# Kernel tuning notes

Hardware: AMD Instinct MI355X
Metric: run time of the kernel (lower is better)

## Reference

```python
import jax, jax.numpy as jnp
import numpy as np

NUM_NODES, NUM_RELS = 100000, 32
VOCAB = NUM_NODES + NUM_RELS
EMB, HID, LAYERS, CW = 128, 768, 4, 3
NHEAD, HDIM = HID // 64, 64
B, S = 4, 1024
T = S - 4 * CW  # rows where the full banded submask fits
EPS = 1e-5


def setup_inputs() -> dict:
    key = jax.random.key(0)
    ks = jax.random.split(key, 24)
    f32 = jnp.float32
    d = {}
    d["seq"] = jax.random.randint(ks[0], (B, S), 0, VOCAB)
    d["neg_ids"] = jax.random.randint(ks[1], (T, B), 0, VOCAB)
    # embedding + LayerNorm
    d["emb_table"] = jax.random.normal(ks[2], (VOCAB, EMB), f32)
    d["emb_ln_g"] = jnp.ones((EMB,), f32)
    d["emb_ln_b"] = jnp.zeros((EMB,), f32)
    # proj: Linear(EMB->HID) + GELU
    d["proj_w"] = jax.random.normal(ks[3], (HID, EMB), f32) * 0.02
    d["proj_b"] = jnp.zeros((HID,), f32)
    # transformer encoder layers (torch post-norm layout)
    d["wqkv"] = jax.random.normal(ks[4], (LAYERS, 3 * HID, HID), f32) * 0.02
    d["bqkv"] = jnp.zeros((LAYERS, 3 * HID), f32)
    d["wo"] = jax.random.normal(ks[5], (LAYERS, HID, HID), f32) * 0.02
    d["bo"] = jnp.zeros((LAYERS, HID), f32)
    d["ln1_g"] = jnp.ones((LAYERS, HID), f32)
    d["ln1_b"] = jnp.zeros((LAYERS, HID), f32)
    d["w1"] = jax.random.normal(ks[6], (LAYERS, 4 * HID, HID), f32) * 0.02
    d["b1"] = jnp.zeros((LAYERS, 4 * HID), f32)
    d["w2"] = jax.random.normal(ks[7], (LAYERS, HID, 4 * HID), f32) * 0.02
    d["b2"] = jnp.zeros((LAYERS, HID), f32)
    d["ln2_g"] = jnp.ones((LAYERS, HID), f32)
    d["ln2_b"] = jnp.zeros((LAYERS, HID), f32)
    # out: Linear(HID->EMB) + LayerNorm
    d["out_w"] = jax.random.normal(ks[8], (EMB, HID), f32) * 0.02
    d["out_b"] = jnp.zeros((EMB,), f32)
    d["out_ln_g"] = jnp.ones((EMB,), f32)
    d["out_ln_b"] = jnp.zeros((EMB,), f32)
    return d


def _ln(x, g, b):
    m = x.mean(-1, keepdims=True)
    v = x.var(-1, keepdims=True)
    return (x - m) * jax.lax.rsqrt(v + EPS) * g + b


def _pos_encoding(s, h):
    pos = jnp.arange(s, dtype=jnp.float32)[:, None]
    div = jnp.exp(jnp.arange(0, h, 2, dtype=jnp.float32) * (-jnp.log(10000.0) / h))
    ang = pos * div  # (S, H/2)
    pe = jnp.zeros((s, h), jnp.float32)
    pe = pe.at[:, 0::2].set(jnp.sin(ang)).at[:, 1::2].set(jnp.cos(ang))
    return pe[:, None, :]  # (S,1,H)


def _band_mask(s):
    i = jnp.arange(s)[:, None]
    j = jnp.arange(s)[None, :]
    gap = j - i
    allowed = (gap >= 0) & (gap <= 4 * CW) & (gap != 2 * CW)
    return jnp.where(allowed, 0.0, -jnp.inf).astype(jnp.float32)


def reference(seq, neg_ids, emb_table, emb_ln_g, emb_ln_b, proj_w, proj_b,
              wqkv, bqkv, wo, bo, ln1_g, ln1_b, w1, b1, w2, b2, ln2_g, ln2_b,
              out_w, out_b, out_ln_g, out_ln_b):
    seq_t = seq.T  # (S,B)
    s, b = seq_t.shape
    z = _ln(emb_table[seq_t], emb_ln_g, emb_ln_b)                 # (S,B,EMB)
    tokens = jax.nn.gelu(jnp.einsum('sbe,he->sbh', z, proj_w) + proj_b,
                         approximate=False)                        # (S,B,HID)
    tokens = tokens + _pos_encoding(s, HID)
    mask = _band_mask(s)                                           # (S,S)
    scale = 1.0 / jnp.sqrt(jnp.float32(HDIM))
    x = tokens
    for l in range(LAYERS):
        qkv = jnp.einsum('sbh,gh->sbg', x, wqkv[l]) + bqkv[l]      # (S,B,3H)
        q, k, v = [t.reshape(s, b, NHEAD, HDIM)
                   for t in jnp.split(qkv, 3, axis=-1)]
        scores = jnp.einsum('sbhd,tbhd->bhst', q, k) * scale + mask
        a = jax.nn.softmax(scores, axis=-1)                        # (B,H,S,S)
        attn = jnp.einsum('bhst,tbhd->sbhd', a, v).reshape(s, b, HID)
        attn = jnp.einsum('sbh,gh->sbg', attn, wo[l]) + bo[l]
        x = _ln(x + attn, ln1_g[l], ln1_b[l])
        ff = jax.nn.gelu(jnp.einsum('sbh,fh->sbf', x, w1[l]) + b1[l],
                         approximate=False)
        ff = jnp.einsum('sbf,hf->sbh', ff, w2[l]) + b2[l]
        x = _ln(x + ff, ln2_g[l], ln2_b[l])
    z_out = _ln(jnp.einsum('sbh,eh->sbe', x, out_w) + out_b,
                out_ln_g, out_ln_b)                                # (S,B,EMB)
    targets = jnp.arange(T) + CW + 1                               # (T,)
    z_hat = z_out[targets]                                         # (T,B,EMB)
    z_pos = z[targets]
    pos = jnp.sum(z_pos * z_hat, axis=-1).reshape(-1)              # (T*B,)
    z_neg = _ln(emb_table[neg_ids], emb_ln_g, emb_ln_b)            # (T,B,EMB)
    neg = jnp.sum(z_neg * z_hat, axis=-1).reshape(-1)              # (T*B,)
    # BCEWithLogitsLoss: labels 1 for pos, 0 for neg
    loss = (jnp.sum(jax.nn.softplus(-pos)) + jnp.sum(jax.nn.softplus(neg))) \
           / (pos.size + neg.size)
    return loss
```

## Files before the change

kernel.cpp:

```cpp
#include <hip/hip_runtime.h>
#include <hip/hip_bf16.h>
#include <math.h>

#define S_LEN 1024
#define B_DIM 4
#define EMB 128
#define HID 768
#define LAYERS 4
#define CW 3
#define NHEAD 12
#define HDIM 64
#define T_LEN (S_LEN - 4*CW)
#define LN_EPS 1e-5f
#define MROWS (S_LEN*B_DIM)

typedef unsigned short u16;
typedef __attribute__((ext_vector_type(8))) __bf16 bf16x8;
typedef __attribute__((ext_vector_type(4))) float f32x4;

__device__ __forceinline__ u16 f2b(float f){
    unsigned u = __float_as_uint(f);
    u += 0x7fff + ((u >> 16) & 1);
    return (u16)(u >> 16);
}
__device__ __forceinline__ float b2f(u16 h){
    return __uint_as_float(((unsigned)h) << 16);
}
__device__ __forceinline__ float gelu_exact(float x){
    return 0.5f * x * (1.0f + erff(x * 0.70710678118654752f));
}
__device__ __forceinline__ float softplus_f(float x){
    return fmaxf(x, 0.0f) + log1pf(expf(-fabsf(x)));
}
template<int N> __device__ __forceinline__ void waitcnt_vm(){
    if constexpr(N==0) asm volatile("s_waitcnt vmcnt(0)" ::: "memory");
    else if constexpr(N==2) asm volatile("s_waitcnt vmcnt(2)" ::: "memory");
    else if constexpr(N==3) asm volatile("s_waitcnt vmcnt(3)" ::: "memory");
    else if constexpr(N==4) asm volatile("s_waitcnt vmcnt(4)" ::: "memory");
    else if constexpr(N==6) asm volatile("s_waitcnt vmcnt(6)" ::: "memory");
    else if constexpr(N==8) asm volatile("s_waitcnt vmcnt(8)" ::: "memory");
}

__global__ void k_cvt(const float* __restrict__ w, u16* __restrict__ o, int n4){
    int i = blockIdx.x*256 + threadIdx.x;
    if(i >= n4) return;
    float4 v = *(const float4*)(w + (size_t)i*4);
    ushort4 t; t.x=f2b(v.x); t.y=f2b(v.y); t.z=f2b(v.z); t.w=f2b(v.w);
    *(ushort4*)(o + (size_t)i*4) = t;
}

__global__ void k_pe(float* __restrict__ pe){
    int idx = blockIdx.x*256 + threadIdx.x;
    if(idx >= S_LEN*HID) return;
    int s = idx / HID, c = idx % HID;
    int i2 = (c >> 1) * 2;
    float freq = expf(-(float)i2 * (logf(10000.0f) / (float)HID));
    float ang = (float)s * freq;
    pe[idx] = (c & 1) ? cosf(ang) : sinf(ang);
}

__global__ void k_embed_ln(const int* __restrict__ seq,
                           const float* __restrict__ emb,
                           const float* __restrict__ g,
                           const float* __restrict__ bta,
                           float* __restrict__ z, u16* __restrict__ zb){
    int row = blockIdx.x;
    int s = row >> 2, b = row & 3;
    int tok = seq[b*S_LEN + s];
    const float* e = emb + (size_t)tok * EMB;
    int lane = threadIdx.x;
    float v0 = e[lane], v1 = e[lane+64];
    float sum = v0+v1, sq = v0*v0+v1*v1;
    #pragma unroll
    for(int off=32; off; off>>=1){ sum += __shfl_xor(sum,off); sq += __shfl_xor(sq,off); }
    float m = sum * (1.0f/128.0f);
    float var = sq*(1.0f/128.0f) - m*m;
    float r = rsqrtf(var + LN_EPS);
    size_t base = (size_t)row*EMB;
    float o0 = (v0-m)*r*g[lane]    + bta[lane];
    float o1 = (v1-m)*r*g[lane+64] + bta[lane+64];
    z[base+lane] = o0; z[base+lane+64] = o1;
    zb[base+lane] = f2b(o0); zb[base+lane+64] = f2b(o1);
}

template<int BM, int BN, int THR, int EPI, int WF, int WB>
__global__ __launch_bounds__(THR) void k_mm(
    const u16*  __restrict__ A,
    const u16*  __restrict__ Bw,
    const float* __restrict__ bias,
    float* __restrict__ Cf, u16* __restrict__ Cb,
    int M, int N, int K, const float* __restrict__ pe)
{
    constexpr int WCOL = (THR==512) ? 4 : 2;
    constexpr int WM = BM/2, WN = BN/WCOL, MR = WM/16, NR = WN/16;
    constexpr int RA = (BM*4)/THR;
    constexpr int RB = (BN*4)/THR;
    constexpr int IC = RA + RB;
    static_assert(RA >= 1 && RB >= 1, "tile too small for THR");
    __shared__ u16 Al[3][BM*32];
    __shared__ u16 Bl[3][BN*32];
    int tid = threadIdx.x;
    int wave = tid >> 6, lane = tid & 63;

    int nbx = N / BN, nby = M / BM, nwg = nbx * nby;
    int bid = blockIdx.x;
    int q = nwg >> 3, rm = nwg & 7, xcd = bid & 7, off = bid >> 3;
    int sbid = (xcd < rm ? xcd*(q+1) : rm*(q+1) + (xcd-rm)*q) + off;
    int row0 = (sbid / nbx) * BM, col0 = (sbid % nbx) * BN;

    int wr = wave / WCOL, wc = wave % WCOL;
    int lr = lane & 15, lk = lane >> 4;

    f32x4 acc[MR][NR];
    #pragma unroll
    for(int m=0;m<MR;m++)
        #pragma unroll
        for(int n=0;n<NR;n++) acc[m][n] = (f32x4){0.f,0.f,0.f,0.f};

    const char* Abase = (const char*)A;
    const char* Bbase = (const char*)Bw;

    auto stage = [&](int buf, int k0){
        #pragma unroll
        for(int i=0;i<RA;i++){
            int p = i*(THR*16) + tid*16;
            int rr = p >> 6, u = (p >> 4) & 3;
            int us = u ^ ((rr >> 1) & 3);
            const char* g = Abase + ((size_t)(row0+rr)*K + k0)*2 + us*16;
            void* l = (char*)&Al[buf][0] + i*(THR*16) + wave*1024;
            __builtin_amdgcn_global_load_lds(
                (const __attribute__((address_space(1))) void*)g,
                (__attribute__((address_space(3))) void*)l, 16, 0, 0);
        }
        #pragma unroll
        for(int i=0;i<RB;i++){
            int p = i*(THR*16) + tid*16;
            int rr = p >> 6, u = (p >> 4) & 3;
            int us = u ^ ((rr >> 1) & 3);
            const char* g = Bbase + ((size_t)(col0+rr)*K + k0)*2 + us*16;
            void* l = (char*)&Bl[buf][0] + i*(THR*16) + wave*1024;
            __builtin_amdgcn_global_load_lds(
                (const __attribute__((address_space(1))) void*)g,
                (__attribute__((address_space(3))) void*)l, 16, 0, 0);
        }
    };

    int nt = K >> 5;
    stage(0, 0);
    if(nt > 1) stage(1, 32);
    int cur = 0;
    for(int t=0; t<nt; ++t){
        int pre = (cur==0) ? 2 : cur-1;
        if(t+2 < nt) stage(pre, (t+2) << 5);
        if(t+2 < nt)      waitcnt_vm<2*IC>();
        else if(t+1 < nt) waitcnt_vm<IC>();
        else              waitcnt_vm<0>();
        __builtin_amdgcn_s_barrier();
        __builtin_amdgcn_sched_barrier(0);
        bf16x8 af[MR], bfr[NR];
        #pragma unroll
        for(int m=0;m<MR;m++){
            int ar = wr*WM + m*16 + lr;
            af[m] = *(const bf16x8*)((const char*)&Al[cur][0] + ar*64 + ((lk ^ ((ar>>1)&3))<<4));
        }
        #pragma unroll
        for(int n=0;n<NR;n++){
            int br = wc*WN + n*16 + lr;
            bfr[n] = *(const bf16x8*)((const char*)&Bl[cur][0] + br*64 + ((lk ^ ((br>>1)&3))<<4));
        }
        #pragma unroll
        for(int m=0;m<MR;m++)
            #pragma unroll
            for(int n=0;n<NR;n++)
                acc[m][n] = __builtin_amdgcn_mfma_f32_16x16x32_bf16(af[m], bfr[n], acc[m][n], 0, 0, 0);
        __builtin_amdgcn_s_barrier();
        cur = (cur==2) ? 0 : cur+1;
    }
    #pragma unroll
    for(int m=0;m<MR;m++){
        #pragma unroll
        for(int n=0;n<NR;n++){
            #pragma unroll
            for(int j=0;j<4;j++){
                int row = row0 + wr*WM + m*16 + lk*4 + j;
                int col = col0 + wc*WN + n*16 + lr;
                float v = acc[m][n][j] + bias[col];
                if(EPI==1) v = gelu_exact(v);
                if(EPI==2) v = gelu_exact(v) + pe[(size_t)(row>>2)*HID + col];
                if(WF) Cf[(size_t)row*N + col] = v;
                if(WB) Cb[(size_t)row*N + col] = f2b(v);
            }
        }
    }
}

__global__ __launch_bounds__(256) void k_attn(const u16* __restrict__ qkv,
                                              u16* __restrict__ out){
    __shared__ float P[4][16][36];
    int wv = threadIdx.x >> 6;
    int lane = threadIdx.x & 63;
    int wid = (blockIdx.x << 2) + wv;
    int h = wid % NHEAD;
    int b = (wid / NHEAD) & 3;
    int s0 = (wid / (NHEAD*B_DIM)) << 4;
    int lr = lane & 15, lk = lane >> 4;
    const int RS = 3*HID;

    bf16x8 qf[2], kf[2][2];
    #pragma unroll
    for(int kk=0;kk<2;kk++)
        qf[kk] = *(const bf16x8*)(qkv + (size_t)((s0+lr)*B_DIM + b)*RS + h*HDIM + kk*32 + lk*8);
    #pragma unroll
    for(int c=0;c<2;c++){
        int t = s0 + c*16 + lr; if(t > S_LEN-1) t = S_LEN-1;
        #pragma unroll
        for(int kk=0;kk<2;kk++)
            kf[c][kk] = *(const bf16x8*)(qkv + (size_t)(t*B_DIM + b)*RS + HID + h*HDIM + kk*32 + lk*8);
    }
    f32x4 acc0 = {0.f,0.f,0.f,0.f}, acc1 = {0.f,0.f,0.f,0.f};
    #pragma unroll
    for(int kk=0;kk<2;kk++){
        acc0 = __builtin_amdgcn_mfma_f32_16x16x32_bf16(qf[kk], kf[0][kk], acc0, 0,0,0);
        acc1 = __builtin_amdgcn_mfma_f32_16x16x32_bf16(qf[kk], kf[1][kk], acc1, 0,0,0);
    }
    float e0[4], e1[4], mx[4], sm[4];
    #pragma unroll
    for(int j=0;j<4;j++){
        int r = 4*lk + j;
        int g0 = lr - r, g1 = 16 + lr - r;
        bool a0 = (g0>=0) & (g0<=12) & (g0!=6);
        bool a1 = (g1>=0) & (g1<=12) & (g1!=6) & (s0+16+lr < S_LEN);
        e0[j] = a0 ? acc0[j]*0.125f : -INFINITY;
        e1[j] = a1 ? acc1[j]*0.125f : -INFINITY;
        mx[j] = fmaxf(e0[j], e1[j]);
    }
    #pragma unroll
    for(int off=1; off<16; off<<=1){
        #pragma unroll
        for(int j=0;j<4;j++) mx[j] = fmaxf(mx[j], __shfl_xor(mx[j], off));
    }
    #pragma unroll
    for(int j=0;j<4;j++){
        e0[j] = expf(e0[j]-mx[j]);
        e1[j] = expf(e1[j]-mx[j]);
        sm[j] = e0[j]+e1[j];
    }
    #pragma unroll
    for(int off=1; off<16; off<<=1){
        #pragma unroll
        for(int j=0;j<4;j++) sm[j] += __shfl_xor(sm[j], off);
    }
    #pragma unroll
    for(int j=0;j<4;j++){
        float inv = 1.0f/sm[j];
        int r = 4*lk + j;
        P[wv][r][lr]      = e0[j]*inv;
        P[wv][r][16+lr]   = e1[j]*inv;
    }
    float o[16];
    #pragma unroll
    for(int r=0;r<16;r++) o[r] = 0.f;
    #pragma unroll
    for(int g4=0; g4<32; g4+=4){
        float vr[4];
        #pragma unroll
        for(int qq=0;qq<4;qq++){
            int t = s0 + g4 + qq; if(t > S_LEN-1) t = S_LEN-1;
            vr[qq] = b2f(qkv[(size_t)(t*B_DIM + b)*RS + 2*HID + h*HDIM + lane]);
        }
        #pragma unroll
        for(int r=0;r<16;r++){
            f32x4 w = *(const f32x4*)&P[wv][r][g4];
            o[r] = fmaf(w[0], vr[0], fmaf(w[1], vr[1], fmaf(w[2], vr[2], fmaf(w[3], vr[3], o[r]))));
        }
    }
    #pragma unroll
    for(int r=0;r<16;r++)
        out[(size_t)((s0+r)*B_DIM + b)*HID + h*HDIM + lane] = f2b(o[r]);
}

__global__ __launch_bounds__(192) void k_add_ln768(
    u16* __restrict__ xb, const u16* __restrict__ y,
    const float* __restrict__ g, const float* __restrict__ bta)
{
    int row = blockIdx.x;
    size_t base = (size_t)row * HID;
    int tid = threadIdx.x;
    int c = tid * 4;
    ushort4 xv = *(const ushort4*)(xb + base + c);
    ushort4 yv = *(const ushort4*)(y  + base + c);
    float v0 = b2f(xv.x)+b2f(yv.x), v1 = b2f(xv.y)+b2f(yv.y);
    float v2 = b2f(xv.z)+b2f(yv.z), v3 = b2f(xv.w)+b2f(yv.w);
    float sum = v0+v1+v2+v3;
    float sq  = v0*v0+v1*v1+v2*v2+v3*v3;
    #pragma unroll
    for(int off=32; off; off>>=1){ sum+=__shfl_xor(sum,off); sq+=__shfl_xor(sq,off); }
    __shared__ float s1[3], s2[3];
    int w = tid>>6;
    if((tid&63)==0){ s1[w]=sum; s2[w]=sq; }
    __syncthreads();
    sum = s1[0]+s1[1]+s1[2];
    sq  = s2[0]+s2[1]+s2[2];
    float m = sum*(1.f/768.f);
    float var = sq*(1.f/768.f) - m*m;
    float r = rsqrtf(var+LN_EPS);
    float4 gv = *(const float4*)(g + c);
    float4 bv = *(const float4*)(bta + c);
    ushort4 o;
    o.x = f2b((v0-m)*r*gv.x + bv.x);
    o.y = f2b((v1-m)*r*gv.y + bv.y);
    o.z = f2b((v2-m)*r*gv.z + bv.z);
    o.w = f2b((v3-m)*r*gv.w + bv.w);
    *(ushort4*)(xb + base + c) = o;
}

__global__ __launch_bounds__(256) void k_loss(
    const float* __restrict__ zout, const float* __restrict__ z,
    const int* __restrict__ neg_ids, const float* __restrict__ emb,
    const float* __restrict__ eg, const float* __restrict__ eb,
    const float* __restrict__ og, const float* __restrict__ ob,
    float* __restrict__ loss)
{
    int wv = threadIdx.x >> 6, lane = threadIdx.x & 63;
    int it0 = blockIdx.x*16 + wv*4;
    float h0r[4], h1r[4], z0[4], z1[4], ee0[4], ee1[4];
    #pragma unroll
    for(int i=0;i<4;i++){
        int it = it0 + i;
        int t = it >> 2, b = it & 3;
        int s = t + CW + 1;
        size_t hb = (size_t)(s*B_DIM+b)*EMB;
        h0r[i] = zout[hb+lane]; h1r[i] = zout[hb+lane+64];
        z0[i]  = z[hb+lane];    z1[i]  = z[hb+lane+64];
        int nid = neg_ids[it];
        const float* e = emb + (size_t)nid*EMB;
        ee0[i] = e[lane]; ee1[i] = e[lane+64];
    }
    float local = 0.f;
    #pragma unroll
    for(int i=0;i<4;i++){
        float hsum = h0r[i]+h1r[i], hsq = h0r[i]*h0r[i]+h1r[i]*h1r[i];
        float esum = ee0[i]+ee1[i], esq = ee0[i]*ee0[i]+ee1[i]*ee1[i];
        #pragma unroll
        for(int off=32; off; off>>=1){
            hsum += __shfl_xor(hsum,off);
            hsq  += __shfl_xor(hsq,off);
            esum += __shfl_xor(esum,off);
            esq  += __shfl_xor(esq,off);
        }
        float hm = hsum*(1.f/128.f), hvar = hsq*(1.f/128.f)-hm*hm, hr = rsqrtf(hvar+LN_EPS);
        float h0 = (h0r[i]-hm)*hr*og[lane]    + ob[lane];
        float h1 = (h1r[i]-hm)*hr*og[lane+64] + ob[lane+64];
        float em = esum*(1.f/128.f), evar = esq*(1.f/128.f)-em*em, er = rsqrtf(evar+LN_EPS);
        float zn0 = (ee0[i]-em)*er*eg[lane]    + eb[lane];
        float zn1 = (ee1[i]-em)*er*eg[lane+64] + eb[lane+64];
        float pv = z0[i]*h0 + z1[i]*h1;
        float nv = zn0*h0 + zn1*h1;
        #pragma unroll
        for(int off=32; off; off>>=1){
            pv += __shfl_xor(pv,off);
            nv += __shfl_xor(nv,off);
        }
        if(lane==0) local += softplus_f(-pv) + softplus_f(nv);
    }
    __shared__ float ls[4];
    if(lane==0) ls[wv] = local;
    __syncthreads();
    if(threadIdx.x==0){
        float v = ls[0]+ls[1]+ls[2]+ls[3];
        atomicAdd(loss, v * (1.0f/(2.0f*T_LEN*B_DIM)));
    }
}

static inline int cvt_grid(size_t n){ return (int)((n/4 + 255)/256); }

extern "C" void kernel_launch(void* const* d_in, const int* in_sizes, int n_in,
                              void* d_out, int out_size, void* d_ws, size_t ws_size,
                              hipStream_t stream) {
    const int*   seq      = (const int*)  d_in[0];
    const int*   neg_ids  = (const int*)  d_in[1];
    const float* emb      = (const float*)d_in[2];
    const float* emb_ln_g = (const float*)d_in[3];
    const float* emb_ln_b = (const float*)d_in[4];
    const float* proj_w   = (const float*)d_in[5];
    const float* proj_b   = (const float*)d_in[6];
    const float* wqkv     = (const float*)d_in[7];
    const float* bqkv     = (const float*)d_in[8];
    const float* wo       = (const float*)d_in[9];
    const float* bo       = (const float*)d_in[10];
    const float* ln1_g    = (const float*)d_in[11];
    const float* ln1_b    = (const float*)d_in[12];
    const float* w1       = (const float*)d_in[13];
    const float* b1       = (const float*)d_in[14];
    const float* w2       = (const float*)d_in[15];
    const float* b2       = (const float*)d_in[16];
    const float* ln2_g    = (const float*)d_in[17];
    const float* ln2_b    = (const float*)d_in[18];
    const float* out_w    = (const float*)d_in[19];
    const float* out_b    = (const float*)d_in[20];
    const float* out_ln_g = (const float*)d_in[21];
    const float* out_ln_b = (const float*)d_in[22];

    const size_t NPROJ = (size_t)HID*EMB;
    const size_t NQKV  = (size_t)3*HID*HID;
    const size_t NWO   = (size_t)HID*HID;
    const size_t NW1   = (size_t)4*HID*HID;
    const size_t NW2   = (size_t)4*HID*HID;
    const size_t NOUT  = (size_t)EMB*HID;

    char* p = (char*)d_ws;
    float* pe   = (float*)p; p += (size_t)S_LEN*HID*4;
    float* z    = (float*)p; p += (size_t)MROWS*EMB*4;
    float* zout = (float*)p; p += (size_t)MROWS*EMB*4;
    u16*  z_b   = (u16*)p;   p += (size_t)MROWS*EMB*2;
    u16*  x_b   = (u16*)p;   p += (size_t)MROWS*HID*2;
    u16*  at_b  = (u16*)p;   p += (size_t)MROWS*HID*2;
    u16*  y_b   = (u16*)p;   p += (size_t)MROWS*HID*2;
    u16*  big   = (u16*)p;   p += (size_t)MROWS*3072*2;
    size_t act_bytes = (size_t)(p - (char*)d_ws);

    size_t full_w_elems = NPROJ + NOUT + LAYERS*(NQKV + NWO + NW1 + NW2);
    bool full = ws_size >= act_bytes + full_w_elems*2;
    size_t fb_elems = NPROJ + NOUT + NQKV + NWO + NW1 + NW2;
    if(!full && ws_size < act_bytes + fb_elems*2) return;

    u16* wbase = (u16*)p;
    u16 *wp_proj, *wp_out, *wp_qkv0, *wp_wo0, *wp_w10, *wp_w20;
    size_t sq, so, s1o, s2o;
    if(full){
        u16* q0 = wbase;
        wp_proj = q0;                 q0 += NPROJ;
        wp_out  = q0;                 q0 += NOUT;
        wp_qkv0 = q0;                 q0 += LAYERS*NQKV;
        wp_wo0  = q0;                 q0 += LAYERS*NWO;
        wp_w10  = q0;                 q0 += LAYERS*NW1;
        wp_w20  = q0;                 q0 += LAYERS*NW2;
        sq = NQKV; so = NWO; s1o = NW1; s2o = NW2;
    } else {
        u16* q0 = wbase;
        wp_proj = q0;                 q0 += NPROJ;
        wp_out  = q0;                 q0 += NOUT;
        wp_qkv0 = q0;                 q0 += NQKV;
        wp_wo0  = q0;                 q0 += NWO;
        wp_w10  = q0;                 q0 += NW1;
        wp_w20  = q0;                 q0 += NW2;
        sq = so = s1o = s2o = 0;
    }

    hipMemsetAsync(d_out, 0, sizeof(float), stream);

    k_pe<<<(S_LEN*HID+255)/256, 256, 0, stream>>>(pe);
    k_embed_ln<<<MROWS, 64, 0, stream>>>(seq, emb, emb_ln_g, emb_ln_b, z, z_b);

    k_cvt<<<cvt_grid(NPROJ), 256, 0, stream>>>(proj_w, wp_proj, (int)(NPROJ/4));
    k_cvt<<<cvt_grid(NOUT),  256, 0, stream>>>(out_w,  wp_out,  (int)(NOUT/4));
    if(full){
        k_cvt<<<cvt_grid(LAYERS*NQKV), 256, 0, stream>>>(wqkv, wp_qkv0, (int)(LAYERS*NQKV/4));
        k_cvt<<<cvt_grid(LAYERS*NWO),  256, 0, stream>>>(wo,   wp_wo0,  (int)(LAYERS*NWO/4));
        k_cvt<<<cvt_grid(LAYERS*NW1),  256, 0, stream>>>(w1,   wp_w10,  (int)(LAYERS*NW1/4));
        k_cvt<<<cvt_grid(LAYERS*NW2),  256, 0, stream>>>(w2,   wp_w20,  (int)(LAYERS*NW2/4));
    }

    k_mm<128,64,256,2,0,1><<<(768/64)*(MROWS/128), 256, 0, stream>>>(
        z_b, wp_proj, proj_b, nullptr, x_b, MROWS, HID, EMB, pe);

    for(int l=0; l<LAYERS; ++l){
        if(!full){
            k_cvt<<<cvt_grid(NQKV), 256, 0, stream>>>(wqkv + (size_t)l*NQKV, wp_qkv0, (int)(NQKV/4));
            k_cvt<<<cvt_grid(NWO),  256, 0, stream>>>(wo   + (size_t)l*NWO,  wp_wo0,  (int)(NWO/4));
            k_cvt<<<cvt_grid(NW1),  256, 0, stream>>>(w1   + (size_t)l*NW1,  wp_w10,  (int)(NW1/4));
            k_cvt<<<cvt_grid(NW2),  256, 0, stream>>>(w2   + (size_t)l*NW2,  wp_w20,  (int)(NW2/4));
        }
        k_mm<128,128,512,0,0,1><<<(2304/128)*(MROWS/128), 512, 0, stream>>>(
            x_b, wp_qkv0 + (size_t)l*sq, bqkv + l*2304, nullptr, big, MROWS, 2304, HID, nullptr);
        k_attn<<<(S_LEN/16)*B_DIM*NHEAD/4, 256, 0, stream>>>(big, at_b);
        k_mm<128,64,256,0,0,1><<<(768/64)*(MROWS/128), 256, 0, stream>>>(
            at_b, wp_wo0 + (size_t)l*so, bo + l*HID, nullptr, y_b, MROWS, HID, HID, nullptr);
        k_add_ln768<<<MROWS, 192, 0, stream>>>(x_b, y_b, ln1_g + l*HID, ln1_b + l*HID);
        k_mm<128,128,512,1,0,1><<<(3072/128)*(MROWS/128), 512, 0, stream>>>(
            x_b, wp_w10 + (size_t)l*s1o, b1 + l*3072, nullptr, big, MROWS, 3072, HID, nullptr);
        k_mm<128,64,256,0,0,1><<<(768/64)*(MROWS/128), 256, 0, stream>>>(
            big, wp_w20 + (size_t)l*s2o, b2 + l*HID, nullptr, y_b, MROWS, HID, 3072, nullptr);
        k_add_ln768<<<MROWS, 192, 0, stream>>>(x_b, y_b, ln2_g + l*HID, ln2_b + l*HID);
    }
    k_mm<64,64,256,0,1,0><<<(EMB/64)*(MROWS/64), 256, 0, stream>>>(
        x_b, wp_out, out_b, zout, nullptr, MROWS, EMB, HID, nullptr);
    k_loss<<<(T_LEN*B_DIM)/16, 256, 0, stream>>>(zout, z, neg_ids, emb,
                                                 emb_ln_g, emb_ln_b, out_ln_g, out_ln_b,
                                                 (float*)d_out);
}
```

Measured before the change: 635.6 us.

## Split-K the FFN down-projection with atomic fp32 accumulation into residual LN

The w2 GEMM (K=3072) now splits K in two, launching twice as many workgroups, each accumulating its partial tile into an fp32 buffer with atomicAdd. The buffer is zeroed with a memset before each FFN, and the bias is added later inside the add+LayerNorm kernel. The Wo projection now also writes fp32 instead of bf16, so the LN kernel reads fp32 residual inputs. The aim is to fill the GPU better on a tall-K GEMM that had only 384 tiles. The cost is atomic traffic, an extra memset per layer, doubled bytes for the intermediate, and non-deterministic summation order.

```diff
diff --git a/kernel.cpp b/kernel.cpp
--- a/kernel.cpp
+++ b/kernel.cpp
@@ -83,7 +83,7 @@
     zb[base+lane] = f2b(o0); zb[base+lane+64] = f2b(o1);
 }
 
-template<int BM, int BN, int THR, int EPI, int WF, int WB>
+template<int BM, int BN, int THR, int SK, int EPI, int WF, int WB>
 __global__ __launch_bounds__(THR) void k_mm(
     const u16*  __restrict__ A,
     const u16*  __restrict__ Bw,
@@ -102,11 +102,14 @@
     int tid = threadIdx.x;
     int wave = tid >> 6, lane = tid & 63;
 
-    int nbx = N / BN, nby = M / BM, nwg = nbx * nby;
+    int nbx = N / BN, nby = M / BM, nwg = nbx * nby * SK;
     int bid = blockIdx.x;
     int q = nwg >> 3, rm = nwg & 7, xcd = bid & 7, off = bid >> 3;
     int sbid = (xcd < rm ? xcd*(q+1) : rm*(q+1) + (xcd-rm)*q) + off;
-    int row0 = (sbid / nbx) * BM, col0 = (sbid % nbx) * BN;
+    int slice = sbid / (nbx*nby);
+    int rb2 = sbid % (nbx*nby);
+    int row0 = (rb2 / nbx) * BM, col0 = (rb2 % nbx) * BN;
+    int kb = slice * (K / SK);
 
     int wr = wave / WCOL, wc = wave % WCOL;
     int lr = lane & 15, lk = lane >> 4;
@@ -145,13 +148,13 @@
         }
     };
 
-    int nt = K >> 5;
-    stage(0, 0);
-    if(nt > 1) stage(1, 32);
+    int nt = (K / SK) >> 5;
+    stage(0, kb);
+    if(nt > 1) stage(1, kb + 32);
     int cur = 0;
     for(int t=0; t<nt; ++t){
         int pre = (cur==0) ? 2 : cur-1;
-        if(t+2 < nt) stage(pre, (t+2) << 5);
+        if(t+2 < nt) stage(pre, kb + ((t+2) << 5));
         if(t+2 < nt)      waitcnt_vm<2*IC>();
         else if(t+1 < nt) waitcnt_vm<IC>();
         else              waitcnt_vm<0>();
@@ -184,11 +187,16 @@
             for(int j=0;j<4;j++){
                 int row = row0 + wr*WM + m*16 + lk*4 + j;
                 int col = col0 + wc*WN + n*16 + lr;
-                float v = acc[m][n][j] + bias[col];
+                float v = acc[m][n][j];
+                if constexpr(EPI!=3) v += bias[col];
                 if(EPI==1) v = gelu_exact(v);
                 if(EPI==2) v = gelu_exact(v) + pe[(size_t)(row>>2)*HID + col];
-                if(WF) Cf[(size_t)row*N + col] = v;
-                if(WB) Cb[(size_t)row*N + col] = f2b(v);
+                if constexpr(EPI==3){
+                    atomicAdd(Cf + (size_t)row*N + col, v);
+                } else {
+                    if(WF) Cf[(size_t)row*N + col] = v;
+                    if(WB) Cb[(size_t)row*N + col] = f2b(v);
+                }
             }
         }
     }
@@ -280,7 +288,8 @@
 }
 
 __global__ __launch_bounds__(192) void k_add_ln768(
-    u16* __restrict__ xb, const u16* __restrict__ y,
+    u16* __restrict__ xb, const float* __restrict__ y,
+    const float* __restrict__ ybias,
     const float* __restrict__ g, const float* __restrict__ bta)
 {
     int row = blockIdx.x;
@@ -288,9 +297,13 @@
     int tid = threadIdx.x;
     int c = tid * 4;
     ushort4 xv = *(const ushort4*)(xb + base + c);
-    ushort4 yv = *(const ushort4*)(y  + base + c);
-    float v0 = b2f(xv.x)+b2f(yv.x), v1 = b2f(xv.y)+b2f(yv.y);
-    float v2 = b2f(xv.z)+b2f(yv.z), v3 = b2f(xv.w)+b2f(yv.w);
+    float4 ya = *(const float4*)(y + base + c);
+    if(ybias){
+        float4 bb = *(const float4*)(ybias + c);
+        ya.x += bb.x; ya.y += bb.y; ya.z += bb.z; ya.w += bb.w;
+    }
+    float v0 = b2f(xv.x)+ya.x, v1 = b2f(xv.y)+ya.y;
+    float v2 = b2f(xv.z)+ya.z, v3 = b2f(xv.w)+ya.w;
     float sum = v0+v1+v2+v3;
     float sq  = v0*v0+v1*v1+v2*v2+v3*v3;
     #pragma unroll
@@ -415,7 +428,7 @@
     u16*  z_b   = (u16*)p;   p += (size_t)MROWS*EMB*2;
     u16*  x_b   = (u16*)p;   p += (size_t)MROWS*HID*2;
     u16*  at_b  = (u16*)p;   p += (size_t)MROWS*HID*2;
-    u16*  y_b   = (u16*)p;   p += (size_t)MROWS*HID*2;
+    float* yf   = (float*)p; p += (size_t)MROWS*HID*4;
     u16*  big   = (u16*)p;   p += (size_t)MROWS*3072*2;
     size_t act_bytes = (size_t)(p - (char*)d_ws);
 
@@ -461,7 +474,7 @@
         k_cvt<<<cvt_grid(LAYERS*NW2),  256, 0, stream>>>(w2,   wp_w20,  (int)(LAYERS*NW2/4));
     }
 
-    k_mm<128,64,256,2,0,1><<<(768/64)*(MROWS/128), 256, 0, stream>>>(
+    k_mm<128,64,256,1,2,0,1><<<(768/64)*(MROWS/128), 256, 0, stream>>>(
         z_b, wp_proj, proj_b, nullptr, x_b, MROWS, HID, EMB, pe);
 
     for(int l=0; l<LAYERS; ++l){
@@ -471,19 +484,20 @@
             k_cvt<<<cvt_grid(NW1),  256, 0, stream>>>(w1   + (size_t)l*NW1,  wp_w10,  (int)(NW1/4));
             k_cvt<<<cvt_grid(NW2),  256, 0, stream>>>(w2   + (size_t)l*NW2,  wp_w20,  (int)(NW2/4));
         }
-        k_mm<128,128,512,0,0,1><<<(2304/128)*(MROWS/128), 512, 0, stream>>>(
+        k_mm<128,128,512,1,0,0,1><<<(2304/128)*(MROWS/128), 512, 0, stream>>>(
             x_b, wp_qkv0 + (size_t)l*sq, bqkv + l*2304, nullptr, big, MROWS, 2304, HID, nullptr);
         k_attn<<<(S_LEN/16)*B_DIM*NHEAD/4, 256, 0, stream>>>(big, at_b);
-        k_mm<128,64,256,0,0,1><<<(768/64)*(MROWS/128), 256, 0, stream>>>(
-            at_b, wp_wo0 + (size_t)l*so, bo + l*HID, nullptr, y_b, MROWS, HID, HID, nullptr);
-        k_add_ln768<<<MROWS, 192, 0, stream>>>(x_b, y_b, ln1_g + l*HID, ln1_b + l*HID);
-        k_mm<128,128,512,1,0,1><<<(3072/128)*(MROWS/128), 512, 0, stream>>>(
+        k_mm<128,64,256,1,0,1,0><<<(768/64)*(MROWS/128), 256, 0, stream>>>(
+            at_b, wp_wo0 + (size_t)l*so, bo + l*HID, yf, nullptr, MROWS, HID, HID, nullptr);
+        k_add_ln768<<<MROWS, 192, 0, stream>>>(x_b, yf, nullptr, ln1_g + l*HID, ln1_b + l*HID);
+        hipMemsetAsync(yf, 0, (size_t)MROWS*HID*4, stream);
+        k_mm<128,128,512,1,1,0,1><<<(3072/128)*(MROWS/128), 512, 0, stream>>>(
             x_b, wp_w10 + (size_t)l*s1o, b1 + l*3072, nullptr, big, MROWS, 3072, HID, nullptr);
-        k_mm<128,64,256,0,0,1><<<(768/64)*(MROWS/128), 256, 0, stream>>>(
-            big, wp_w20 + (size_t)l*s2o, b2 + l*HID, nullptr, y_b, MROWS, HID, 3072, nullptr);
-        k_add_ln768<<<MROWS, 192, 0, stream>>>(x_b, y_b, ln2_g + l*HID, ln2_b + l*HID);
-    }
-    k_mm<64,64,256,0,1,0><<<(EMB/64)*(MROWS/64), 256, 0, stream>>>(
+        k_mm<128,64,256,2,3,0,0><<<(768/64)*(MROWS/128)*2, 256, 0, stream>>>(
+            big, wp_w20 + (size_t)l*s2o, nullptr, yf, nullptr, MROWS, HID, 3072, nullptr);
+        k_add_ln768<<<MROWS, 192, 0, stream>>>(x_b, yf, b2 + l*HID, ln2_g + l*HID, ln2_b + l*HID);
+    }
+    k_mm<64,64,256,1,0,1,0><<<(EMB/64)*(MROWS/64), 256, 0, stream>>>(
         x_b, wp_out, out_b, zout, nullptr, MROWS, EMB, HID, nullptr);
     k_loss<<<(T_LEN*B_DIM)/16, 256, 0, stream>>>(zout, z, neg_ids, emb,
                                                  emb_ln_g, emb_ln_b, out_ln_g, out_ln_b,
```

New measurement: 687.2 us. 1.08x slower.
